# Kernel tuning notes

Hardware: AMD Instinct MI355X
Metric: run time of the kernel (lower is better)

The kernel has to match this reference:

```python
import jax, jax.numpy as jnp
import numpy as np

EMB_DIM = 1024
NUM_HEADS = 16
HEAD_DIM = EMB_DIM // NUM_HEADS


def setup_inputs() -> dict:
    key = jax.random.key(0)
    ks = jax.random.split(key, 9)
    B, S = 2, 2048
    s = 1.0 / np.sqrt(EMB_DIM)
    return {
        "x": jax.random.normal(ks[0], (B, S, EMB_DIM), jnp.float32),
        "Wq": jax.random.normal(ks[1], (EMB_DIM, EMB_DIM), jnp.float32) * s,
        "bq": jnp.zeros((EMB_DIM,), jnp.float32),
        "Wk": jax.random.normal(ks[2], (EMB_DIM, EMB_DIM), jnp.float32) * s,
        "bk": jnp.zeros((EMB_DIM,), jnp.float32),
        "Wv": jax.random.normal(ks[3], (EMB_DIM, EMB_DIM), jnp.float32) * s,
        "bv": jnp.zeros((EMB_DIM,), jnp.float32),
        "Wo": jax.random.normal(ks[4], (EMB_DIM, EMB_DIM), jnp.float32) * s,
        "bo": jnp.zeros((EMB_DIM,), jnp.float32),
    }


def reference(x, Wq, bq, Wk, bk, Wv, bv, Wo, bo):
    B, S, E = x.shape
    H, D = NUM_HEADS, HEAD_DIM
    # QKV projections (torch Linear: x @ W.T + b; here W is stored as [in,out])
    q = (x @ Wq + bq).reshape(B, S, H, D).transpose(0, 2, 1, 3)  # [B,H,S,D]
    k = (x @ Wk + bk).reshape(B, S, H, D).transpose(0, 2, 1, 3)
    v = (x @ Wv + bv).reshape(B, S, H, D).transpose(0, 2, 1, 3)
    # raw scores, then causal mask with -inf, then scale inside softmax
    scores = jnp.einsum("bhqd,bhkd->bhqk", q, k)  # [B,H,S,S]
    causal = jnp.tril(jnp.ones((S, S), bool))
    scores = jnp.where(causal, scores, -jnp.inf)
    attn = jax.nn.softmax(scores / np.sqrt(D), axis=-1)
    # dropout prob is 0.0 (eval-equivalent), so it's identity
    ctx = jnp.einsum("bhqk,bhkd->bhqd", attn, v)  # [B,H,S,D]
    ctx = ctx.transpose(0, 2, 1, 3).reshape(B, S, E)
    return ctx @ Wo + bo
```

## Files before the change

### kernel.cpp

```cpp
#include <hip/hip_runtime.h>
#include <hip/hip_bf16.h>
#include <cstdint>

#define NB   2
#define NS   2048
#define NE   1024
#define NH   16
#define ND   64
#define BS   (NB*NS)

typedef float f32x4 __attribute__((ext_vector_type(4)));
typedef __bf16 bf16x8 __attribute__((ext_vector_type(8)));

#define MFMA16(a,b,c) __builtin_amdgcn_mfma_f32_16x16x32_bf16((a),(b),(c),0,0,0)

#define KCF 0.18033688011112042f

typedef const __attribute__((address_space(1))) unsigned int* gas_u32;
typedef __attribute__((address_space(3))) unsigned int* las_u32;

__device__ __forceinline__ void gload_lds16(const void* g, void* l) {
    __builtin_amdgcn_global_load_lds((gas_u32)g, (las_u32)l, 16, 0, 0);
}

__device__ __forceinline__ unsigned short bf16_bits(float f) {
    __bf16 h = (__bf16)f;
    return __builtin_bit_cast(unsigned short, h);
}
__device__ __forceinline__ float bits_bf16(unsigned short u) {
    return (float)__builtin_bit_cast(__bf16, u);
}

__global__ __launch_bounds__(256) void convx_kernel(const float* __restrict__ x,
                                                    __bf16* __restrict__ xb) {
    size_t i = ((size_t)blockIdx.x * 256 + threadIdx.x) * 8;
    const float4* p = (const float4*)(x + i);
    float4 a = p[0], c = p[1];
    bf16x8 v;
    v[0]=(__bf16)a.x; v[1]=(__bf16)a.y; v[2]=(__bf16)a.z; v[3]=(__bf16)a.w;
    v[4]=(__bf16)c.x; v[5]=(__bf16)c.y; v[6]=(__bf16)c.z; v[7]=(__bf16)c.w;
    *(bf16x8*)(xb + i) = v;
}

__global__ __launch_bounds__(256) void wtrans_kernel(const float* __restrict__ W0,
                                                     const float* __restrict__ W1,
                                                     const float* __restrict__ W2,
                                                     const float* __restrict__ W3,
                                                     __bf16* __restrict__ wt) {
    __shared__ float tile[32][33];
    int z = blockIdx.z;
    const float* W = (z==0) ? W0 : (z==1) ? W1 : (z==2) ? W2 : W3;
    __bf16* out = wt + (size_t)z * NE * NE;
    int tx = threadIdx.x, ty = threadIdx.y;
    int k0 = blockIdx.y * 32, n0 = blockIdx.x * 32;
    #pragma unroll
    for (int i = 0; i < 4; i++)
        tile[ty + 8*i][tx] = W[(size_t)(k0 + ty + 8*i) * NE + n0 + tx];
    __syncthreads();
    #pragma unroll
    for (int i = 0; i < 4; i++)
        out[(size_t)(n0 + ty + 8*i) * NE + k0 + tx] = (__bf16)tile[tx][ty + 8*i];
}

template<int EPI>
__global__ __launch_bounds__(256, 2) void gemm128_kernel(
        const __bf16* __restrict__ A, const __bf16* __restrict__ Bt,
        const float* __restrict__ bias0, const float* __restrict__ bias1,
        const float* __restrict__ bias2,
        __bf16* __restrict__ o0, __bf16* __restrict__ o1, __bf16* __restrict__ o2,
        float* __restrict__ fout) {
    __shared__ char smem[16384];
    const int K = 1024;
    int t = threadIdx.x;
    int wave = t >> 6, lane = t & 63;
    int wm = wave >> 1, wn = wave & 1;
    int lg = lane >> 4, li = lane & 15;
    int m0 = blockIdx.y * 128, n0 = blockIdx.x * 128;

    const __bf16* Ag = A + (size_t)(m0 + (t >> 2)) * K + (t & 3) * 8;
    const __bf16* Bg = Bt + (size_t)(n0 + (t >> 2)) * K + (t & 3) * 8;

    f32x4 acc[4][4] = {};

    for (int k0 = 0; k0 < K; k0 += 32) {
        __syncthreads();
        gload_lds16(Ag + k0,          smem +         t * 16);
        gload_lds16(Ag + 64 * K + k0, smem +  4096 + t * 16);
        gload_lds16(Bg + k0,          smem +  8192 + t * 16);
        gload_lds16(Bg + 64 * K + k0, smem + 12288 + t * 16);
        __syncthreads();

        const __bf16* As = (const __bf16*)smem;
        const __bf16* Bs = (const __bf16*)(smem + 8192);
        bf16x8 af[4], bfr[4];
        #pragma unroll
        for (int i = 0; i < 4; i++)
            af[i] = *(const bf16x8*)(As + (size_t)(wm*64 + i*16 + li) * 32 + lg * 8);
        #pragma unroll
        for (int i = 0; i < 4; i++)
            bfr[i] = *(const bf16x8*)(Bs + (size_t)(wn*64 + i*16 + li) * 32 + lg * 8);
        #pragma unroll
        for (int i = 0; i < 4; i++)
            #pragma unroll
            for (int j = 0; j < 4; j++)
                acc[i][j] = MFMA16(af[i], bfr[j], acc[i][j]);
    }

    #pragma unroll
    for (int i = 0; i < 4; i++) {
        int mrow = m0 + wm * 64 + i * 16 + lg * 4;
        #pragma unroll
        for (int j = 0; j < 4; j++) {
            int n = n0 + wn * 64 + j * 16 + li;
            if (EPI == 0) {
                int widx = n >> 10, nn = n & 1023;
                const float* bb = (widx == 0) ? bias0 : (widx == 1) ? bias1 : bias2;
                __bf16* dst = (widx == 0) ? o0 : (widx == 1) ? o1 : o2;
                float bv = bb[nn];
                float scl = (widx == 0) ? KCF : 1.0f;
                int h = nn >> 6, d = nn & 63;
                #pragma unroll
                for (int r = 0; r < 4; r++) {
                    int m = mrow + r;
                    int bidx = m >> 11, s = m & 2047;
                    dst[(((size_t)bidx * NH + h) * NS + s) * ND + d] =
                        (__bf16)((acc[i][j][r] + bv) * scl);
                }
            } else {
                float bv = bias0[n];
                #pragma unroll
                for (int r = 0; r < 4; r++)
                    fout[(size_t)(mrow + r) * NE + n] = acc[i][j][r] + bv;
            }
        }
    }
}

__global__ __launch_bounds__(256) void vtrans_kernel(const __bf16* __restrict__ vb,
                                                     __bf16* __restrict__ vt) {
    __shared__ __bf16 tile[32][33];
    int bh = blockIdx.z;
    int s0 = blockIdx.x * 32, d0 = blockIdx.y * 32;
    const __bf16* src = vb + (size_t)bh * NS * ND;
    __bf16* dst = vt + (size_t)bh * ND * NS;
    int tx = threadIdx.x, ty = threadIdx.y;
    #pragma unroll
    for (int i = 0; i < 4; i++)
        tile[ty + 8*i][tx] = src[(size_t)(s0 + ty + 8*i) * ND + d0 + tx];
    __syncthreads();
    #pragma unroll
    for (int i = 0; i < 4; i++)
        dst[(size_t)(d0 + ty + 8*i) * NS + s0 + tx] = tile[tx][ty + 8*i];
}

__global__ __launch_bounds__(256) void attn_kernel(const __bf16* __restrict__ qb,
                                                   const __bf16* __restrict__ kb,
                                                   const __bf16* __restrict__ vt,
                                                   __bf16* __restrict__ ctx,
                                                   __bf16* __restrict__ Opart,
                                                   float* __restrict__ lbuf,
                                                   int split) {
    __shared__ __align__(16) char kbuf[2][8192];
    __shared__ __align__(16) char vbuf[2][8192];
    __shared__ __align__(16) ushort pbuf[4][1024];

    int t = threadIdx.x;
    int wave = t >> 6, lane = t & 63;
    int lg = lane >> 4, li = lane & 15;
    int bh = blockIdx.y, b = bh >> 4, h = bh & 15;
    int bx = blockIdx.x;

    int qt, c, nch;
    if (!split) {
        qt = bx; c = 0; nch = 1;
    } else {
        int a = (bx < 8) ? 0 : (bx < 24) ? 1 : (bx < 48) ? 2 : 3;
        int seg = (a == 0) ? 0 : (a == 1) ? 8 : (a == 2) ? 24 : 48;
        int idx = bx - seg;
        int dv = a + 1;
        qt = a * 8 + idx / dv;
        c  = idx % dv;
        nch = a + 1;
    }
    int jlo = c * 8;
    int jhi = min(jlo + 8, qt + 1);
    int nt = jhi - jlo;
    bool direct = (nch == 1);

    int qw = qt * 64 + wave * 16;
    const __bf16* Q  = qb + ((size_t)bh * NS + qw) * ND;
    const __bf16* Kg = kb + (size_t)bh * NS * ND;
    const __bf16* Vg = vt + (size_t)bh * ND * NS;

    int sr = t >> 3;
    int sg = (t & 7) ^ (sr & 7);
    const __bf16* Ks0 = Kg + (size_t)sr * ND + sg * 8;
    const __bf16* Ks1 = Kg + (size_t)(32 + sr) * ND + sg * 8;
    const __bf16* Vs0 = Vg + (size_t)sr * NS + sg * 8;
    const __bf16* Vs1 = Vg + (size_t)(32 + sr) * NS + sg * 8;

#define STAGE_KV(J, BI) do {                                              \
        gload_lds16(Ks0 + (size_t)(J) * 4096, &kbuf[BI][t * 16]);         \
        gload_lds16(Ks1 + (size_t)(J) * 4096, &kbuf[BI][4096 + t * 16]);  \
        gload_lds16(Vs0 + (size_t)(J) * 64,   &vbuf[BI][t * 16]);         \
        gload_lds16(Vs1 + (size_t)(J) * 64,   &vbuf[BI][4096 + t * 16]);  \
    } while (0)

    bf16x8 aq0 = *(const bf16x8*)(Q + li * ND + lg * 8);
    bf16x8 aq1 = *(const bf16x8*)(Q + li * ND + 32 + lg * 8);

    STAGE_KV(jlo, 0);

    f32x4 o[4] = {};
    float lpart = 0.f;
    int swz = (li & 7) << 4;
    int qg = qw + li;

    char* pw = (char*)&pbuf[wave][0];
    char* pwr = pw + li * 128 + (lg & 1) * 8;
    int k6base = (lg >> 1);

    __syncthreads();

    for (int it = 0; it < nt; ++it) {
        int j = jlo + it;
        int cur = it & 1;
        if (it + 1 < nt) STAGE_KV(j + 1, cur ^ 1);

        const char* kt = (const char*)kbuf[cur];
        f32x4 sc[4];
        #pragma unroll
        for (int h4 = 0; h4 < 4; ++h4) {
            const char* kr = kt + (h4 * 16 + li) * 128;
            bf16x8 b0 = *(const bf16x8*)(kr + ((lg << 4) ^ swz));
            bf16x8 b1 = *(const bf16x8*)(kr + (((4 + lg) << 4) ^ swz));
            f32x4 z = {};
            z = MFMA16(b0, aq0, z);
            z = MFMA16(b1, aq1, z);
            sc[h4] = z;
        }

        if (j == qt) {
            #pragma unroll
            for (int h4 = 0; h4 < 4; ++h4)
                #pragma unroll
                for (int r = 0; r < 4; ++r) {
                    int kv = j * 64 + h4 * 16 + lg * 4 + r;
                    if (kv > qg) sc[h4][r] = -1e30f;
                }
        }

        #pragma unroll
        for (int h4 = 0; h4 < 4; ++h4) {
            #pragma unroll
            for (int r = 0; r < 4; ++r) {
                float p = exp2f(sc[h4][r]);
                sc[h4][r] = p;
                lpart += p;
            }
        }

        #pragma unroll
        for (int h4 = 0; h4 < 4; ++h4) {
            uint2 w64;
            w64.x = (unsigned int)bf16_bits(sc[h4][0]) |
                    ((unsigned int)bf16_bits(sc[h4][1]) << 16);
            w64.y = (unsigned int)bf16_bits(sc[h4][2]) |
                    ((unsigned int)bf16_bits(sc[h4][3]) << 16);
            int k6 = h4 * 2 + k6base;
            *(uint2*)(pwr + (((k6 ^ (li & 7)) << 4))) = w64;
        }
        asm volatile("s_waitcnt lgkmcnt(0)" ::: "memory");

        const char* vtl = (const char*)vbuf[cur];
        #pragma unroll
        for (int ks = 0; ks < 2; ++ks) {
            int ch = (ks * 4 + lg) << 4;
            bf16x8 pf = *(const bf16x8*)(pw + li * 128 + (ch ^ swz));
            #pragma unroll
            for (int i = 0; i < 4; ++i) {
                bf16x8 vf = *(const bf16x8*)(vtl + (i * 16 + li) * 128 + (ch ^ swz));
                o[i] = MFMA16(vf, pf, o[i]);
            }
        }
        __syncthreads();
    }
#undef STAGE_KV

    float lsum = lpart + __shfl_xor(lpart, 16);
    lsum += __shfl_xor(lsum, 32);

    if (direct) {
        float inv = 1.f / lsum;
        __bf16* dst = ctx + ((size_t)b * NS + qg) * NE + h * ND;
        #pragma unroll
        for (int i = 0; i < 4; ++i) {
            ushort4 pack;
            pack.x = bf16_bits(o[i][0] * inv);
            pack.y = bf16_bits(o[i][1] * inv);
            pack.z = bf16_bits(o[i][2] * inv);
            pack.w = bf16_bits(o[i][3] * inv);
            *(ushort4*)(dst + i * 16 + lg * 4) = pack;
        }
    } else {
        int slot = bh * 80 + bx;
        int ql = wave * 16 + li;
        __bf16* Op = Opart + (size_t)slot * 4096 + ql * 64;
        #pragma unroll
        for (int i = 0; i < 4; ++i) {
            ushort4 pack;
            pack.x = bf16_bits(o[i][0]);
            pack.y = bf16_bits(o[i][1]);
            pack.z = bf16_bits(o[i][2]);
            pack.w = bf16_bits(o[i][3]);
            *(ushort4*)(Op + i * 16 + lg * 4) = pack;
        }
        if (lg == 0)
            lbuf[(size_t)slot * 64 + ql] = lsum;
    }
}

__global__ __launch_bounds__(256) void combine_kernel(const __bf16* __restrict__ Opart,
                                                      const float* __restrict__ lbuf,
                                                      __bf16* __restrict__ ctx) {
    int qt = 8 + blockIdx.x;
    int bh = blockIdx.y, b = bh >> 4, h = bh & 15;
    int a = qt >> 3, bq = qt & 7;
    int off = (a + 1) * (4 * a + bq);
    int nch = a + 1;
    int slotbase = bh * 80 + off;
    int t = threadIdx.x;
    int q = t >> 2, dg = t & 3;

    float L = 0.f;
    #pragma unroll
    for (int c = 0; c < 4; ++c)
        if (c < nch)
            L += lbuf[(size_t)(slotbase + c) * 64 + q];
    float invL = 1.f / L;

    float acc[16] = {};
    #pragma unroll
    for (int c = 0; c < 4; ++c)
        if (c < nch) {
            const uint4* src = (const uint4*)(Opart + (size_t)(slotbase + c) * 4096 +
                                              q * 64 + dg * 16);
            #pragma unroll
            for (int half = 0; half < 2; ++half) {
                uint4 v = src[half];
                unsigned int w[4] = {v.x, v.y, v.z, v.w};
                #pragma unroll
                for (int u = 0; u < 4; ++u) {
                    acc[half * 8 + u * 2]     += bits_bf16((ushort)(w[u] & 0xffff));
                    acc[half * 8 + u * 2 + 1] += bits_bf16((ushort)(w[u] >> 16));
                }
            }
        }

    int qg = qt * 64 + q;
    __bf16* dst = ctx + ((size_t)b * NS + qg) * NE + h * ND + dg * 16;
    #pragma unroll
    for (int half = 0; half < 2; ++half) {
        ushort4 pack;
        pack.x = bf16_bits(acc[half * 8 + 0] * invL);
        pack.y = bf16_bits(acc[half * 8 + 1] * invL);
        pack.z = bf16_bits(acc[half * 8 + 2] * invL);
        pack.w = bf16_bits(acc[half * 8 + 3] * invL);
        ushort4 pack2;
        pack2.x = bf16_bits(acc[half * 8 + 4] * invL);
        pack2.y = bf16_bits(acc[half * 8 + 5] * invL);
        pack2.z = bf16_bits(acc[half * 8 + 6] * invL);
        pack2.w = bf16_bits(acc[half * 8 + 7] * invL);
        *(ushort4*)(dst + half * 8) = pack;
        *(ushort4*)(dst + half * 8 + 4) = pack2;
    }
}

extern "C" void kernel_launch(void* const* d_in, const int* in_sizes, int n_in,
                              void* d_out, int out_size, void* d_ws, size_t ws_size,
                              hipStream_t stream) {
    (void)in_sizes; (void)n_in; (void)out_size;
    const float* x  = (const float*)d_in[0];
    const float* Wq = (const float*)d_in[1];
    const float* bq = (const float*)d_in[2];
    const float* Wk = (const float*)d_in[3];
    const float* bk = (const float*)d_in[4];
    const float* Wv = (const float*)d_in[5];
    const float* bv = (const float*)d_in[6];
    const float* Wo = (const float*)d_in[7];
    const float* bo = (const float*)d_in[8];
    float* out = (float*)d_out;

    char* ws = (char*)d_ws;
    const size_t MB = 1024 * 1024;
    __bf16* xb  = (__bf16*)(ws);
    __bf16* wt  = (__bf16*)(ws +  8 * MB);
    __bf16* qb  = (__bf16*)(ws + 16 * MB);
    __bf16* kb  = (__bf16*)(ws + 24 * MB);
    __bf16* vb  = (__bf16*)(ws + 32 * MB);
    __bf16* vtb = (__bf16*)(ws + 40 * MB);
    __bf16* ctx = xb;
    __bf16* Opart = (__bf16*)(ws + 48 * MB);
    float*  lbuf  = (float*)(ws + 48 * MB + 20971520);
    const size_t NEED = 48 * MB + 20971520 + 655360;

    int split = (ws_size >= NEED) ? 1 : 0;

    convx_kernel<<<(BS * NE) / (256 * 8), 256, 0, stream>>>(x, xb);
    wtrans_kernel<<<dim3(32, 32, 4), dim3(32, 8), 0, stream>>>(Wq, Wk, Wv, Wo, wt);
    gemm128_kernel<0><<<dim3(24, 32), 256, 0, stream>>>(
        xb, wt, bq, bk, bv, qb, kb, vb, nullptr);
    vtrans_kernel<<<dim3(NS / 32, ND / 32, NB * NH), dim3(32, 8), 0, stream>>>(vb, vtb);
    attn_kernel<<<dim3(split ? 80 : 32, NB * NH), 256, 0, stream>>>(
        qb, kb, vtb, ctx, Opart, lbuf, split);
    if (split)
        combine_kernel<<<dim3(24, NB * NH), 256, 0, stream>>>(Opart, lbuf, ctx);
    gemm128_kernel<1><<<dim3(8, 32), 256, 0, stream>>>(
        ctx, wt + 3 * MB, bo, nullptr, nullptr, nullptr, nullptr, nullptr, out);
}
```

Measured before the change: 208.3 us.

## Fuse prep kernels, double-buffer GEMM LDS, write V transposed from GEMM

```diff
diff --git a/kernel.cpp b/kernel.cpp
--- a/kernel.cpp
+++ b/kernel.cpp
@@ -31,27 +31,33 @@
     return (float)__builtin_bit_cast(__bf16, u);
 }
 
-__global__ __launch_bounds__(256) void convx_kernel(const float* __restrict__ x,
-                                                    __bf16* __restrict__ xb) {
-    size_t i = ((size_t)blockIdx.x * 256 + threadIdx.x) * 8;
-    const float4* p = (const float4*)(x + i);
-    float4 a = p[0], c = p[1];
-    bf16x8 v;
-    v[0]=(__bf16)a.x; v[1]=(__bf16)a.y; v[2]=(__bf16)a.z; v[3]=(__bf16)a.w;
-    v[4]=(__bf16)c.x; v[5]=(__bf16)c.y; v[6]=(__bf16)c.z; v[7]=(__bf16)c.w;
-    *(bf16x8*)(xb + i) = v;
-}
-
-__global__ __launch_bounds__(256) void wtrans_kernel(const float* __restrict__ W0,
-                                                     const float* __restrict__ W1,
-                                                     const float* __restrict__ W2,
-                                                     const float* __restrict__ W3,
-                                                     __bf16* __restrict__ wt) {
+__global__ __launch_bounds__(256) void prep_kernel(const float* __restrict__ x,
+                                                   __bf16* __restrict__ xb,
+                                                   const float* __restrict__ W0,
+                                                   const float* __restrict__ W1,
+                                                   const float* __restrict__ W2,
+                                                   const float* __restrict__ W3,
+                                                   __bf16* __restrict__ wt) {
     __shared__ float tile[32][33];
     int z = blockIdx.z;
-    const float* W = (z==0) ? W0 : (z==1) ? W1 : (z==2) ? W2 : W3;
-    __bf16* out = wt + (size_t)z * NE * NE;
     int tx = threadIdx.x, ty = threadIdx.y;
+    if (z == 0) {
+        size_t base = ((size_t)(blockIdx.y * 32 + blockIdx.x) * 256 +
+                       ty * 32 + tx) * 16;
+        const float4* p = (const float4*)(x + base);
+        float4 a = p[0], b = p[1], c = p[2], d = p[3];
+        bf16x8 v0, v1;
+        v0[0]=(__bf16)a.x; v0[1]=(__bf16)a.y; v0[2]=(__bf16)a.z; v0[3]=(__bf16)a.w;
+        v0[4]=(__bf16)b.x; v0[5]=(__bf16)b.y; v0[6]=(__bf16)b.z; v0[7]=(__bf16)b.w;
+        v1[0]=(__bf16)c.x; v1[1]=(__bf16)c.y; v1[2]=(__bf16)c.z; v1[3]=(__bf16)c.w;
+        v1[4]=(__bf16)d.x; v1[5]=(__bf16)d.y; v1[6]=(__bf16)d.z; v1[7]=(__bf16)d.w;
+        *(bf16x8*)(xb + base) = v0;
+        *(bf16x8*)(xb + base + 8) = v1;
+        return;
+    }
+    int w = z - 1;
+    const float* W = (w==0) ? W0 : (w==1) ? W1 : (w==2) ? W2 : W3;
+    __bf16* out = wt + (size_t)w * NE * NE;
     int k0 = blockIdx.y * 32, n0 = blockIdx.x * 32;
     #pragma unroll
     for (int i = 0; i < 4; i++)
@@ -69,7 +75,7 @@
         const float* __restrict__ bias2,
         __bf16* __restrict__ o0, __bf16* __restrict__ o1, __bf16* __restrict__ o2,
         float* __restrict__ fout) {
-    __shared__ char smem[16384];
+    __shared__ __align__(16) char smem[2][16384];
     const int K = 1024;
     int t = threadIdx.x;
     int wave = t >> 6, lane = t & 63;
@@ -80,18 +86,23 @@
     const __bf16* Ag = A + (size_t)(m0 + (t >> 2)) * K + (t & 3) * 8;
     const __bf16* Bg = Bt + (size_t)(n0 + (t >> 2)) * K + (t & 3) * 8;
 
+#define GSTAGE(K0, BI) do {                                             \
+        gload_lds16(Ag + (K0),          smem[BI] +         t * 16);     \
+        gload_lds16(Ag + 64 * K + (K0), smem[BI] +  4096 + t * 16);     \
+        gload_lds16(Bg + (K0),          smem[BI] +  8192 + t * 16);     \
+        gload_lds16(Bg + 64 * K + (K0), smem[BI] + 12288 + t * 16);     \
+    } while (0)
+
+    GSTAGE(0, 0);
     f32x4 acc[4][4] = {};
+    __syncthreads();
 
     for (int k0 = 0; k0 < K; k0 += 32) {
-        __syncthreads();
-        gload_lds16(Ag + k0,          smem +         t * 16);
-        gload_lds16(Ag + 64 * K + k0, smem +  4096 + t * 16);
-        gload_lds16(Bg + k0,          smem +  8192 + t * 16);
-        gload_lds16(Bg + 64 * K + k0, smem + 12288 + t * 16);
-        __syncthreads();
-
-        const __bf16* As = (const __bf16*)smem;
-        const __bf16* Bs = (const __bf16*)(smem + 8192);
+        int cur = (k0 >> 5) & 1;
+        if (k0 + 32 < K) GSTAGE(k0 + 32, cur ^ 1);
+
+        const __bf16* As = (const __bf16*)smem[cur];
+        const __bf16* Bs = (const __bf16*)(smem[cur] + 8192);
         bf16x8 af[4], bfr[4];
         #pragma unroll
         for (int i = 0; i < 4; i++)
@@ -104,7 +115,10 @@
             #pragma unroll
             for (int j = 0; j < 4; j++)
                 acc[i][j] = MFMA16(af[i], bfr[j], acc[i][j]);
-    }
+
+        __syncthreads();
+    }
+#undef GSTAGE
 
     #pragma unroll
     for (int i = 0; i < 4; i++) {
@@ -115,16 +129,23 @@
             if (EPI == 0) {
                 int widx = n >> 10, nn = n & 1023;
                 const float* bb = (widx == 0) ? bias0 : (widx == 1) ? bias1 : bias2;
-                __bf16* dst = (widx == 0) ? o0 : (widx == 1) ? o1 : o2;
                 float bv = bb[nn];
-                float scl = (widx == 0) ? KCF : 1.0f;
                 int h = nn >> 6, d = nn & 63;
-                #pragma unroll
-                for (int r = 0; r < 4; r++) {
-                    int m = mrow + r;
-                    int bidx = m >> 11, s = m & 2047;
-                    dst[(((size_t)bidx * NH + h) * NS + s) * ND + d] =
-                        (__bf16)((acc[i][j][r] + bv) * scl);
+                int bidx = mrow >> 11, s0 = mrow & 2047;
+                if (widx == 2) {
+                    ushort4 pk;
+                    pk.x = bf16_bits(acc[i][j][0] + bv);
+                    pk.y = bf16_bits(acc[i][j][1] + bv);
+                    pk.z = bf16_bits(acc[i][j][2] + bv);
+                    pk.w = bf16_bits(acc[i][j][3] + bv);
+                    *(ushort4*)(o2 + (((size_t)bidx * NH + h) * ND + d) * NS + s0) = pk;
+                } else {
+                    __bf16* dst = (widx == 0) ? o0 : o1;
+                    float scl = (widx == 0) ? KCF : 1.0f;
+                    #pragma unroll
+                    for (int r = 0; r < 4; r++)
+                        dst[(((size_t)bidx * NH + h) * NS + s0 + r) * ND + d] =
+                            (__bf16)((acc[i][j][r] + bv) * scl);
                 }
             } else {
                 float bv = bias0[n];
@@ -134,23 +155,6 @@
             }
         }
     }
-}
-
-__global__ __launch_bounds__(256) void vtrans_kernel(const __bf16* __restrict__ vb,
-                                                     __bf16* __restrict__ vt) {
-    __shared__ __bf16 tile[32][33];
-    int bh = blockIdx.z;
-    int s0 = blockIdx.x * 32, d0 = blockIdx.y * 32;
-    const __bf16* src = vb + (size_t)bh * NS * ND;
-    __bf16* dst = vt + (size_t)bh * ND * NS;
-    int tx = threadIdx.x, ty = threadIdx.y;
-    #pragma unroll
-    for (int i = 0; i < 4; i++)
-        tile[ty + 8*i][tx] = src[(size_t)(s0 + ty + 8*i) * ND + d0 + tx];
-    __syncthreads();
-    #pragma unroll
-    for (int i = 0; i < 4; i++)
-        dst[(size_t)(d0 + ty + 8*i) * NS + s0 + tx] = tile[tx][ty + 8*i];
 }
 
 __global__ __launch_bounds__(256) void attn_kernel(const __bf16* __restrict__ qb,
@@ -397,24 +401,23 @@
     __bf16* wt  = (__bf16*)(ws +  8 * MB);
     __bf16* qb  = (__bf16*)(ws + 16 * MB);
     __bf16* kb  = (__bf16*)(ws + 24 * MB);
-    __bf16* vb  = (__bf16*)(ws + 32 * MB);
-    __bf16* vtb = (__bf16*)(ws + 40 * MB);
+    __bf16* vtb = (__bf16*)(ws + 32 * MB);
     __bf16* ctx = xb;
-    __bf16* Opart = (__bf16*)(ws + 48 * MB);
-    float*  lbuf  = (float*)(ws + 48 * MB + 20971520);
-    const size_t NEED = 48 * MB + 20971520 + 655360;
+    __bf16* Opart = (__bf16*)(ws + 40 * MB);
+    float*  lbuf  = (float*)(ws + 40 * MB + 20971520);
+    const size_t NEED = 40 * MB + 20971520 + 655360;
 
     int split = (ws_size >= NEED) ? 1 : 0;
 
-    convx_kernel<<<(BS * NE) / (256 * 8), 256, 0, stream>>>(x, xb);
-    wtrans_kernel<<<dim3(32, 32, 4), dim3(32, 8), 0, stream>>>(Wq, Wk, Wv, Wo, wt);
+    prep_kernel<<<dim3(32, 32, 5), dim3(32, 8), 0, stream>>>(
+        x, xb, Wq, Wk, Wv, Wo, wt);
     gemm128_kernel<0><<<dim3(24, 32), 256, 0, stream>>>(
-        xb, wt, bq, bk, bv, qb, kb, vb, nullptr);
-    vtrans_kernel<<<dim3(NS / 32, ND / 32, NB * NH), dim3(32, 8), 0, stream>>>(vb, vtb);
+        xb, wt, bq, bk, bv, qb, kb, vtb, nullptr);
     attn_kernel<<<dim3(split ? 80 : 32, NB * NH), 256, 0, stream>>>(
         qb, kb, vtb, ctx, Opart, lbuf, split);
     if (split)
         combine_kernel<<<dim3(24, NB * NH), 256, 0, stream>>>(Opart, lbuf, ctx);
     gemm128_kernel<1><<<dim3(8, 32), 256, 0, stream>>>(
-        ctx, wt + 3 * MB, bo, nullptr, nullptr, nullptr, nullptr, nullptr, out);
-}
+        ctx, wt + 3 * (size_t)NE * NE, bo, nullptr, nullptr, nullptr, nullptr,
+        nullptr, out);
+}
```

Result: faster. 193.6 us (-7.1%).
